# Performance work log

Measured on AMD Instinct MI355X. Metric: run time of the kernel, lower is better.

Reference implementation:

```python
import jax, jax.numpy as jnp
import numpy as np

D = 512
H = 4
HD = D // H
FF = 4 * D
B = 512
T = 128
EMA_K = 128
LOC_K = 4
DECAY = 0.9
STEP = 0.5 / np.sqrt(128 / 32)  # 0.25
EPS = 1e-5


def layernorm(x, g, b):
    mu = jnp.mean(x, axis=-1, keepdims=True)
    var = jnp.mean(jnp.square(x - mu), axis=-1, keepdims=True)
    return (x - mu) * jax.lax.rsqrt(var + EPS) * g + b


def dwconv_causal(x, w):
    # x: (B,T,D), w: (D,K); torch Conv1d(groups=D, padding=K-1) sliced to [:T]
    K = w.shape[1]
    xt = jnp.transpose(x, (0, 2, 1))  # (B,D,T)
    y = jax.lax.conv_general_dilated(
        xt, w[:, None, :], window_strides=(1,), padding=[(K - 1, 0)],
        feature_group_count=x.shape[-1], dimension_numbers=('NCT', 'OIT', 'NCT'))
    return jnp.transpose(y, (0, 2, 1))


def rope(qk, cos, sin):
    # qk: (B,H,T,HD)
    x1, x2 = jnp.split(qk, 2, axis=-1)
    rot = jnp.concatenate([-x2, x1], axis=-1)
    return qk * cos + rot * sin


def setup_inputs() -> dict:
    key = jax.random.key(0)
    ks = jax.random.split(key, 24)
    s = 0.02
    inp = {
        'parallel_repr': jax.random.normal(ks[0], (B, T, D), jnp.float32),
        'sequential_state': jax.random.normal(ks[1], (B, D), jnp.float32),
        'q_w': jax.random.normal(ks[2], (D, D), jnp.float32) * s,
        'q_b': jnp.zeros((D,), jnp.float32),
        'k_w': jax.random.normal(ks[3], (D, D), jnp.float32) * s,
        'k_b': jnp.zeros((D,), jnp.float32),
        'v_w': jax.random.normal(ks[4], (D, D), jnp.float32) * s,
        'v_b': jnp.zeros((D,), jnp.float32),
        'o_w': jax.random.normal(ks[5], (D, D), jnp.float32) * s,
        'o_b': jnp.zeros((D,), jnp.float32),
        'local_w': jax.random.normal(ks[6], (D, LOC_K), jnp.float32) * 0.1,
        'local_b': jax.random.normal(ks[7], (D,), jnp.float32) * 0.1,
        'delta_w': jax.random.normal(ks[8], (3 * D, D), jnp.float32) * s,
        'delta_b': jnp.zeros((D,), jnp.float32),
        'gate_w': jax.random.normal(ks[9], (3 * D, D), jnp.float32) * s,
        'gate_b': jnp.zeros((D,), jnp.float32),
        'dn_g': jnp.ones((D,), jnp.float32), 'dn_b': jnp.zeros((D,), jnp.float32),
        'ln1_g': jnp.ones((D,), jnp.float32), 'ln1_b': jnp.zeros((D,), jnp.float32),
        'ln2_g': jnp.ones((D,), jnp.float32), 'ln2_b': jnp.zeros((D,), jnp.float32),
        'ln3_g': jnp.ones((D,), jnp.float32), 'ln3_b': jnp.zeros((D,), jnp.float32),
        'ln4_g': jnp.ones((D,), jnp.float32), 'ln4_b': jnp.zeros((D,), jnp.float32),
        'seq_w': jax.random.normal(ks[10], (D, D), jnp.float32) * s,
        'seq_b': jnp.zeros((D,), jnp.float32),
        'ffn_w1': jax.random.normal(ks[11], (D, FF), jnp.float32) * s,
        'ffn_b1': jnp.zeros((FF,), jnp.float32),
        'ffn_w2': jax.random.normal(ks[12], (FF, D), jnp.float32) * s,
        'ffn_b2': jnp.zeros((D,), jnp.float32),
    }
    # EMA kernel: coefficient (1-d)*d^lag on x[t-lag]; stored flipped as in torch
    ema = (1.0 - DECAY) * DECAY ** jnp.arange(EMA_K, dtype=jnp.float32)
    inp['ema_w'] = jnp.broadcast_to(ema[::-1][None, :], (D, EMA_K))
    return inp


def reference(parallel_repr, sequential_state, q_w, q_b, k_w, k_b, v_w, v_b,
              o_w, o_b, local_w, local_b, delta_w, delta_b, gate_w, gate_b,
              dn_g, dn_b, ln1_g, ln1_b, ln2_g, ln2_b, ln3_g, ln3_b, ln4_g, ln4_b,
              seq_w, seq_b, ffn_w1, ffn_b1, ffn_w2, ffn_b2, ema_w):
    x = parallel_repr
    Bb, Tt, Dd = x.shape
    # --- RoPE causal attention ---
    inv_freq = 1.0 / (10000.0 ** (jnp.arange(0, HD, 2, dtype=jnp.float32) / HD))
    t = jnp.arange(Tt, dtype=jnp.float32)
    freqs = jnp.outer(t, inv_freq)                      # (T, HD/2)
    emb = jnp.concatenate([freqs, freqs], axis=-1)      # (T, HD)
    cos = jnp.cos(emb)[None, None]
    sin = jnp.sin(emb)[None, None]
    def heads(y):
        return jnp.transpose(y.reshape(Bb, Tt, H, HD), (0, 2, 1, 3))
    q = rope(heads(x @ q_w + q_b), cos, sin)
    k = rope(heads(x @ k_w + k_b), cos, sin)
    v = heads(x @ v_w + v_b)
    scores = jnp.einsum('bhtd,bhsd->bhts', q, k) / np.sqrt(HD)
    causal = jnp.tril(jnp.ones((Tt, Tt), dtype=bool))
    scores = jnp.where(causal, scores, jnp.float32(-1e9))
    attn = jax.nn.softmax(scores, axis=-1)
    attn_out = jnp.einsum('bhts,bhsd->bhtd', attn, v)
    attn_out = jnp.transpose(attn_out, (0, 2, 1, 3)).reshape(Bb, Tt, Dd)
    attn_out = attn_out @ o_w + o_b
    x1 = layernorm(x + attn_out, ln1_g, ln1_b)
    # --- depthwise causal convs ---
    local_hist = dwconv_causal(x1, local_w) + local_b
    global_sum = dwconv_causal(x1, ema_w)
    combined = jnp.concatenate([x1, local_hist, global_sum], axis=-1)  # (B,T,3D)
    deltas = jax.nn.sigmoid(combined @ gate_w + gate_b) * jnp.tanh(combined @ delta_w + delta_b)
    deltas = layernorm(deltas, dn_g, dn_b)
    acc = jnp.cumsum(deltas, axis=1) * STEP
    states = layernorm(sequential_state[:, None, :] + acc, ln3_g, ln3_b)
    seq_guidance = states @ seq_w + seq_b
    ffn_in = x1 + 0.3 * seq_guidance
    h = jax.nn.gelu(ffn_in @ ffn_w1 + ffn_b1, approximate=False)
    ffn_out = h @ ffn_w2 + ffn_b2
    out = layernorm(x1 + ffn_out, ln2_g, ln2_b)
    final_state = layernorm(states[:, -1, :], ln4_g, ln4_b)
    return out, final_state
```

## Files before the change

kernel.cpp:

```cpp
#include <hip/hip_runtime.h>
#include <cstddef>
#include <cstdint>

#define BB   512
#define TT   128
#define DD   512
#define HH   4
#define HDIM 128
#define FFD  2048
#define NROWS (BB * TT)
#define SLOT ((size_t)NROWS * DD)

typedef unsigned short u16;
typedef __bf16 bf16x8 __attribute__((ext_vector_type(8)));
typedef float  f32x4  __attribute__((ext_vector_type(4)));

__device__ __forceinline__ u16 f2b(float x) {
    union { float f; unsigned u; } v; v.f = x;
    unsigned r = v.u + 0x7FFFu + ((v.u >> 16) & 1u);
    return (u16)(r >> 16);
}
__device__ __forceinline__ float b2f(u16 u) {
    union { unsigned u; float f; } v; v.u = (unsigned)u << 16; return v.f;
}
__device__ __forceinline__ float fast_gelu(float v) {
    float t = v * (0.7978845608028654f + 0.0356774081f * v * v);
    float e = __expf(2.f * t);
    float th = 1.f - 2.f / (e + 1.f);
    return 0.5f * v * (1.f + th);
}
__device__ __forceinline__ void glds16(const void* g, void* l) {
    __builtin_amdgcn_global_load_lds(
        (const __attribute__((address_space(1))) void*)g,
        (__attribute__((address_space(3))) void*)l, 16, 0, 0);
}

template<int MODE>
__global__ __launch_bounds__(256)
void gemm128(const u16* __restrict__ A, const u16* __restrict__ BT,
             const float* __restrict__ bias, void* __restrict__ Cout, int ldc,
             const float* __restrict__ addsrc, void* __restrict__ aux,
             int K, int M)
{
    __shared__ u16 S[16384];
    const int tid = threadIdx.x;
    const int gx  = gridDim.x;
    const int nwg = gx * gridDim.y;
    int orig = blockIdx.y * gx + blockIdx.x;
    if ((nwg & 7) == 0) orig = (orig & 7) * (nwg >> 3) + (orig >> 3);
    const int row0 = (orig / gx) * 128;
    const int col0 = (orig % gx) * 128;

    const int lane = tid & 63;
    const int w    = tid >> 6;
    const int wr   = (w >> 1) * 64;
    const int wc   = (w & 1) * 64;
    const int fr   = lane & 15;
    const int kq   = lane >> 4;

    f32x4 acc[4][4];
#pragma unroll
    for (int m = 0; m < 4; ++m)
#pragma unroll
        for (int n = 0; n < 4; ++n) acc[m][n] = (f32x4){0.f, 0.f, 0.f, 0.f};

    const u16* agp[4]; const u16* bgp[4]; int dstoff[4];
#pragma unroll
    for (int j = 0; j < 4; ++j) {
        const int p   = w * 256 + j * 64 + lane;
        const int row = p >> 3;
        const int lc  = (p & 7) ^ (row & 7);
        agp[j] = A  + (size_t)(row0 + row) * K + lc * 8;
        bgp[j] = BT + (size_t)(col0 + row) * K + lc * 8;
        dstoff[j] = p * 8;
    }

    const int NKT = K >> 6;
    for (int kt = 0; kt < NKT; ++kt) {
        const int ko = kt * 64;
#pragma unroll
        for (int j = 0; j < 4; ++j) {
            glds16(agp[j] + ko, S + dstoff[j]);
            glds16(bgp[j] + ko, S + 8192 + dstoff[j]);
        }
        __syncthreads();
#pragma unroll
        for (int kk = 0; kk < 2; ++kk) {
            bf16x8 av[4], bv[4];
#pragma unroll
            for (int m = 0; m < 4; ++m) {
                const int r  = wr + m * 16 + fr;
                const int ch = (kk * 4 + kq) ^ (r & 7);
                av[m] = *(const bf16x8*)(S + r * 64 + ch * 8);
            }
#pragma unroll
            for (int n = 0; n < 4; ++n) {
                const int r  = wc + n * 16 + fr;
                const int ch = (kk * 4 + kq) ^ (r & 7);
                bv[n] = *(const bf16x8*)(S + 8192 + r * 64 + ch * 8);
            }
#pragma unroll
            for (int m = 0; m < 4; ++m)
#pragma unroll
                for (int n = 0; n < 4; ++n)
                    acc[m][n] = __builtin_amdgcn_mfma_f32_16x16x32_bf16(
                        av[m], bv[n], acc[m][n], 0, 0, 0);
        }
        __syncthreads();
    }

    if constexpr (MODE == 7) {
        if (col0 >= 1024) {
#pragma unroll
            for (int m = 0; m < 4; ++m)
#pragma unroll
                for (int j = 0; j < 4; ++j) {
                    const int tl = wr + m * 16 + (lane >> 4) * 4 + j;
#pragma unroll
                    for (int n = 0; n < 4; ++n) {
                        const int dc = wc + n * 16 + fr;
                        float v = acc[m][n][j] + bias[col0 + dc];
                        *(u16*)((char*)S + dc * 256 + ((tl * 2) ^ ((dc & 7) << 4))) = f2b(v);
                    }
                }
            __syncthreads();
            u16* dst = (u16*)aux + ((size_t)((row0 >> 7) * 4 + ((col0 - 1024) >> 7)) << 14);
#pragma unroll
            for (int i = 0; i < 8; ++i)
                *(uint4*)(dst + (size_t)(i * 256 + tid) * 8) =
                    *(const uint4*)((char*)S + (size_t)(i * 256 + tid) * 16);
        } else {
#pragma unroll
            for (int m = 0; m < 4; ++m)
#pragma unroll
                for (int j = 0; j < 4; ++j) {
                    const int r = row0 + wr + m * 16 + (lane >> 4) * 4 + j;
#pragma unroll
                    for (int n = 0; n < 4; ++n) {
                        const int c = col0 + wc + n * 16 + fr;
                        ((u16*)Cout)[(size_t)r * 1024 + c] = f2b(acc[m][n][j] + bias[c]);
                    }
                }
        }
    } else {
#pragma unroll
        for (int m = 0; m < 4; ++m) {
#pragma unroll
            for (int j = 0; j < 4; ++j) {
                const int r = row0 + wr + m * 16 + (lane >> 4) * 4 + j;
#pragma unroll
                for (int n = 0; n < 4; ++n) {
                    const int c = col0 + wc + n * 16 + fr;
                    float v = acc[m][n][j] + bias[c];
                    if constexpr (MODE == 2) {
                        ((u16*)Cout)[(size_t)r * ldc + c] =
                            f2b(addsrc[(size_t)r * M + c] + 0.3f * v);
                    } else if constexpr (MODE == 3) {
                        ((u16*)Cout)[(size_t)r * ldc + c] = f2b(fast_gelu(v));
                    } else if constexpr (MODE == 6) {
                        float pth = __shfl_xor(v, 1);
                        if ((fr & 1) == 0) {
                            float sg = 1.f / (1.f + __expf(-v));
                            float e  = __expf(2.f * pth);
                            float th = 1.f - 2.f / (e + 1.f);
                            ((u16*)Cout)[(size_t)r * ldc + (c >> 1)] = f2b(sg * th);
                        }
                    } else {
                        ((u16*)Cout)[(size_t)r * ldc + c] = f2b(v);
                    }
                }
            }
        }
    }
    (void)aux;
}

__global__ __launch_bounds__(256)
void wtrans_kernel(const float* __restrict__ W, u16* __restrict__ WT, int K, int M,
                   int rmul, int roff)
{
    __shared__ float t[32][33];
    const int m0 = blockIdx.x * 32;
    const int k0 = blockIdx.y * 32;
    const int tx = threadIdx.x;
    const int ty = threadIdx.y;
#pragma unroll
    for (int i = 0; i < 4; ++i) {
        int k = ty * 4 + i;
        t[k][tx] = W[(size_t)(k0 + k) * M + m0 + tx];
    }
    __syncthreads();
#pragma unroll
    for (int i = 0; i < 4; ++i) {
        int m = ty * 4 + i;
        WT[(size_t)((m0 + m) * rmul + roff) * K + k0 + tx] = f2b(t[tx][m]);
    }
}

__global__ void cast_f2b_kernel(const float* __restrict__ in, u16* __restrict__ out, size_t n4)
{
    size_t i = (size_t)blockIdx.x * blockDim.x + threadIdx.x;
    if (i >= n4) return;
    float4 v = reinterpret_cast<const float4*>(in)[i];
    union { u16 u[4]; uint2 d; } p;
    p.u[0] = f2b(v.x); p.u[1] = f2b(v.y); p.u[2] = f2b(v.z); p.u[3] = f2b(v.w);
    reinterpret_cast<uint2*>(out)[i] = p.d;
}

__global__ void rope_table_kernel(float* __restrict__ tabc, float* __restrict__ tabs)
{
    int idx = blockIdx.x * blockDim.x + threadIdx.x;
    if (idx >= TT * 64) return;
    int t = idx >> 6, j = idx & 63;
    float invf = expf(-(float)j * (9.210340371976184f / 64.f));
    float ang  = (float)t * invf;
    tabc[idx] = cosf(ang);
    tabs[idx] = sinf(ang);
}

__global__ void bias_build_kernel(const float* qb, const float* kb, const float* vb,
                                  const float* gb, const float* db,
                                  float* qkvb, float* gdb)
{
    int i = blockIdx.x * blockDim.x + threadIdx.x;
    if (i >= 512) return;
    qkvb[i] = qb[i]; qkvb[512 + i] = kb[i]; qkvb[1024 + i] = vb[i];
    gdb[2 * i] = gb[i]; gdb[2 * i + 1] = db[i];
}

__global__ __launch_bounds__(256)
void attn_mfma_kernel(const u16* __restrict__ QKg, const u16* __restrict__ VTg,
                      u16* __restrict__ Og,
                      const float* __restrict__ tabc, const float* __restrict__ tabs)
{
    __shared__ u16 SA[128 * 128];
    __shared__ u16 SB[128 * 128];
    const int h = blockIdx.x, b = blockIdx.y;
    const int tid  = threadIdx.x;
    const int lane = tid & 63;
    const int w    = tid >> 6;
    const int fr   = lane & 15;
    const int kq   = lane >> 4;
    const size_t baseq = ((size_t)(b * TT)) * 1024 + (size_t)h * HDIM;
    const size_t baseo = ((size_t)(b * TT)) * DD + (size_t)h * HDIM;

    {
        const int tg = tid >> 4;
        const int dg = tid & 15;
        const int j0 = (dg & 7) * 8;
        const bool hi = (dg & 8) != 0;
        for (int r = 0; r < 8; ++r) {
            const int t = r * 16 + tg;
            uint4 qv = *(const uint4*)(QKg + baseq + (size_t)t * 1024 + dg * 8);
            uint4 kv = *(const uint4*)(QKg + baseq + 512 + (size_t)t * 1024 + dg * 8);
            unsigned qa[4] = {qv.x, qv.y, qv.z, qv.w};
            unsigned ka[4] = {kv.x, kv.y, kv.z, kv.w};
            unsigned qb[4], kb[4];
#pragma unroll
            for (int i = 0; i < 4; ++i) {
                qb[i] = __shfl_xor((int)qa[i], 8);
                kb[i] = __shfl_xor((int)ka[i], 8);
            }
            const float* cp = tabc + t * 64 + j0;
            const float* sp = tabs + t * 64 + j0;
            u16 oq[8], ok[8];
#pragma unroll
            for (int e = 0; e < 8; ++e) {
                float fq = b2f((u16)(qa[e >> 1] >> ((e & 1) * 16)));
                float gq = b2f((u16)(qb[e >> 1] >> ((e & 1) * 16)));
                float fk = b2f((u16)(ka[e >> 1] >> ((e & 1) * 16)));
                float gk = b2f((u16)(kb[e >> 1] >> ((e & 1) * 16)));
                float c = cp[e], s = sp[e];
                oq[e] = f2b(hi ? fq * c + gq * s : fq * c - gq * s);
                ok[e] = f2b(hi ? fk * c + gk * s : fk * c - gk * s);
            }
            const int cb = (dg * 16) ^ ((t & 7) << 4);
            *(uint4*)((char*)SA + t * 256 + cb) = *(const uint4*)oq;
            *(uint4*)((char*)SB + t * 256 + cb) = *(const uint4*)ok;
        }
    }
    __syncthreads();

    f32x4 acc[2][8];
#pragma unroll
    for (int m = 0; m < 2; ++m)
#pragma unroll
        for (int n = 0; n < 8; ++n) acc[m][n] = (f32x4){0.f, 0.f, 0.f, 0.f};

    for (int k0 = 0; k0 < 128; k0 += 32) {
        const int cb = (k0 + kq * 8) * 2;
        bf16x8 af[2];
#pragma unroll
        for (int m = 0; m < 2; ++m) {
            const int row = w * 32 + m * 16 + fr;
            af[m] = *(const bf16x8*)((char*)SA + row * 256 + (cb ^ ((row & 7) << 4)));
        }
#pragma unroll
        for (int n = 0; n < 8; ++n) {
            const int row = n * 16 + fr;
            bf16x8 bf = *(const bf16x8*)((char*)SB + row * 256 + (cb ^ ((row & 7) << 4)));
            acc[0][n] = __builtin_amdgcn_mfma_f32_16x16x32_bf16(af[0], bf, acc[0][n], 0, 0, 0);
            acc[1][n] = __builtin_amdgcn_mfma_f32_16x16x32_bf16(af[1], bf, acc[1][n], 0, 0, 0);
        }
    }
    __syncthreads();

    {
        const u16* vsrc = VTg + ((size_t)(b * HH + h) << 14);
#pragma unroll
        for (int i = 0; i < 8; ++i)
            glds16(vsrc + (size_t)(i * 256 + tid) * 8,
                   SB + (size_t)(i * 256 + tid) * 8);
    }

    const float SC = 0.08838834764831845f;
#pragma unroll
    for (int m = 0; m < 2; ++m) {
#pragma unroll
        for (int j = 0; j < 4; ++j) {
            const int t = w * 32 + m * 16 + kq * 4 + j;
            float mx = -3.0e38f;
#pragma unroll
            for (int n = 0; n < 8; ++n) {
                const int s = n * 16 + fr;
                float v = acc[m][n][j];
                v = (s <= t) ? v * SC : -3.0e38f;
                acc[m][n][j] = v;
                mx = fmaxf(mx, v);
            }
            mx = fmaxf(mx, __shfl_xor(mx, 1));
            mx = fmaxf(mx, __shfl_xor(mx, 2));
            mx = fmaxf(mx, __shfl_xor(mx, 4));
            mx = fmaxf(mx, __shfl_xor(mx, 8));
            float sum = 0.f;
#pragma unroll
            for (int n = 0; n < 8; ++n) {
                float e = __expf(acc[m][n][j] - mx);
                acc[m][n][j] = e; sum += e;
            }
            sum += __shfl_xor(sum, 1); sum += __shfl_xor(sum, 2);
            sum += __shfl_xor(sum, 4); sum += __shfl_xor(sum, 8);
            const float inv = 1.f / sum;
#pragma unroll
            for (int n = 0; n < 8; ++n) {
                const int s = n * 16 + fr;
                *(u16*)((char*)SA + t * 256 + ((s * 2) ^ ((t & 7) << 4))) =
                    f2b(acc[m][n][j] * inv);
            }
        }
    }
    __syncthreads();

    f32x4 oa[2][8];
#pragma unroll
    for (int m = 0; m < 2; ++m)
#pragma unroll
        for (int n = 0; n < 8; ++n) oa[m][n] = (f32x4){0.f, 0.f, 0.f, 0.f};

    for (int k0 = 0; k0 < 128; k0 += 32) {
        const int cb = (k0 + kq * 8) * 2;
        bf16x8 pa[2];
#pragma unroll
        for (int m = 0; m < 2; ++m) {
            const int row = w * 32 + m * 16 + fr;
            pa[m] = *(const bf16x8*)((char*)SA + row * 256 + (cb ^ ((row & 7) << 4)));
        }
#pragma unroll
        for (int n = 0; n < 8; ++n) {
            const int row = n * 16 + fr;
            bf16x8 vb = *(const bf16x8*)((char*)SB + row * 256 + (cb ^ ((row & 7) << 4)));
            oa[0][n] = __builtin_amdgcn_mfma_f32_16x16x32_bf16(pa[0], vb, oa[0][n], 0, 0, 0);
            oa[1][n] = __builtin_amdgcn_mfma_f32_16x16x32_bf16(pa[1], vb, oa[1][n], 0, 0, 0);
        }
    }

#pragma unroll
    for (int m = 0; m < 2; ++m)
#pragma unroll
        for (int j = 0; j < 4; ++j) {
            const int t = w * 32 + m * 16 + kq * 4 + j;
            u16* orow = Og + baseo + (size_t)t * DD;
#pragma unroll
            for (int n = 0; n < 8; ++n)
                orow[n * 16 + fr] = f2b(oa[m][n][j]);
        }
}

__device__ __forceinline__ float2 blk_red512(float v, float (*red)[2], int tid)
{
    float s = v, ss = v * v;
#pragma unroll
    for (int off = 1; off < 64; off <<= 1) {
        s  += __shfl_xor(s, off);
        ss += __shfl_xor(ss, off);
    }
    if ((tid & 63) == 0) { red[tid >> 6][0] = s; red[tid >> 6][1] = ss; }
    __syncthreads();
    float S = 0.f, SS = 0.f;
#pragma unroll
    for (int w = 0; w < 8; ++w) { S += red[w][0]; SS += red[w][1]; }
    return make_float2(S, SS);
}

__global__ __launch_bounds__(512)
void ln1_chain_kernel(const float* __restrict__ x, const u16* __restrict__ oo,
                      const float* __restrict__ g, const float* __restrict__ bb,
                      const float* __restrict__ lw, const float* __restrict__ lb,
                      float* __restrict__ X1, u16* __restrict__ Cb)
{
    __shared__ float red[2][8][2];
    const int b = blockIdx.x, d = threadIdx.x;
    const float g_ = g[d], b_ = bb[d];
    const float w0 = lw[d * 4 + 0], w1 = lw[d * 4 + 1],
                w2 = lw[d * 4 + 2], w3 = lw[d * 4 + 3];
    const float lb_ = lb[d];
    const size_t rb = (size_t)b * TT;
    float h1 = 0.f, h2 = 0.f, h3 = 0.f, ema = 0.f;
    float v = x[(rb + 0) * DD + d] + b2f(oo[(rb + 0) * DD + d]);
    for (int t = 0; t < TT; ++t) {
        const int tn = (t < TT - 1) ? t + 1 : t;
        float vn = x[(rb + tn) * DD + d] + b2f(oo[(rb + tn) * DD + d]);
        float2 r = blk_red512(v, red[t & 1], d);
        float mu  = r.x * (1.f / DD);
        float var = r.y * (1.f / DD) - mu * mu;
        float x1v = (v - mu) * rsqrtf(var + 1e-5f) * g_ + b_;
        const size_t row = rb + t;
        X1[row * DD + d] = x1v;
        u16* crow = Cb + row * 1536;
        crow[d] = f2b(x1v);
        crow[512 + d]  = f2b(lb_ + w3 * x1v + w2 * h1 + w1 * h2 + w0 * h3);
        ema = 0.9f * ema + 0.1f * x1v;
        crow[1024 + d] = f2b(ema);
        h3 = h2; h2 = h1; h1 = x1v;
        v = vn;
    }
}

__global__ __launch_bounds__(512)
void state_chain_kernel(const u16* __restrict__ deltasB, const float* __restrict__ seqst,
                        const float* __restrict__ dng, const float* __restrict__ dnb,
                        const float* __restrict__ g3, const float* __restrict__ b3,
                        const float* __restrict__ g4, const float* __restrict__ b4,
                        u16* __restrict__ statesb, float* __restrict__ fstate)
{
    __shared__ float red[2][8][2];
    const int b = blockIdx.x, d = threadIdx.x;
    const float gd_ = dng[d], bd_ = dnb[d], g3_ = g3[d], b3_ = b3[d];
    const float seq = seqst[(size_t)b * DD + d];
    const size_t rb = (size_t)b * TT;
    float cum = 0.f;
    float v = b2f(deltasB[(rb + 0) * DD + d]);
    for (int t = 0; t < TT; ++t) {
        const int tn = (t < TT - 1) ? t + 1 : t;
        float vn = b2f(deltasB[(rb + tn) * DD + d]);
        float2 r0 = blk_red512(v, red[0], d);
        float mu  = r0.x * (1.f / DD);
        float var = r0.y * (1.f / DD) - mu * mu;
        float nd  = (v - mu) * rsqrtf(var + 1e-5f) * gd_ + bd_;
        cum += nd;
        float sv = seq + cum * 0.25f;
        float2 r1 = blk_red512(sv, red[1], d);
        mu  = r1.x * (1.f / DD);
        var = r1.y * (1.f / DD) - mu * mu;
        float o = (sv - mu) * rsqrtf(var + 1e-5f) * g3_ + b3_;
        statesb[(rb + t) * DD + d] = f2b(o);
        if (t == TT - 1) {
            float2 r2 = blk_red512(o, red[0], d);
            float mu4  = r2.x * (1.f / DD);
            float var4 = r2.y * (1.f / DD) - mu4 * mu4;
            fstate[(size_t)b * DD + d] = (o - mu4) * rsqrtf(var4 + 1e-5f) * g4[d] + b4[d];
        }
        v = vn;
    }
}

__global__ __launch_bounds__(256)
void ln2_kernel(const float* __restrict__ a, const u16* __restrict__ badd,
                const float* __restrict__ g, const float* __restrict__ bb,
                float* __restrict__ out)
{
    const int row = blockIdx.x;
    const int tid = threadIdx.x;
    const float* ap = a + (size_t)row * DD;
    const u16*   bp = badd + (size_t)row * DD;
    float v0 = ap[tid]       + b2f(bp[tid]);
    float v1 = ap[tid + 256] + b2f(bp[tid + 256]);
    float s  = v0 + v1;
    float ss = v0 * v0 + v1 * v1;
#pragma unroll
    for (int off = 1; off < 64; off <<= 1) {
        s  += __shfl_xor(s, off);
        ss += __shfl_xor(ss, off);
    }
    __shared__ float sm1[4], sm2[4];
    const int wid = tid >> 6;
    if ((tid & 63) == 0) { sm1[wid] = s; sm2[wid] = ss; }
    __syncthreads();
    s  = sm1[0] + sm1[1] + sm1[2] + sm1[3];
    ss = sm2[0] + sm2[1] + sm2[2] + sm2[3];
    const float mu  = s * (1.f / DD);
    const float var = ss * (1.f / DD) - mu * mu;
    const float r   = rsqrtf(var + 1e-5f);
    float* op = out + (size_t)row * DD;
    op[tid]       = (v0 - mu) * r * g[tid]       + bb[tid];
    op[tid + 256] = (v1 - mu) * r * g[tid + 256] + bb[tid + 256];
}

extern "C" void kernel_launch(void* const* d_in, const int* in_sizes, int n_in,
                              void* d_out, int out_size, void* d_ws, size_t ws_size,
                              hipStream_t stream)
{
    const float* x       = (const float*)d_in[0];
    const float* seqst   = (const float*)d_in[1];
    const float* q_w     = (const float*)d_in[2];
    const float* q_b     = (const float*)d_in[3];
    const float* k_w     = (const float*)d_in[4];
    const float* k_b     = (const float*)d_in[5];
    const float* v_w     = (const float*)d_in[6];
    const float* v_b     = (const float*)d_in[7];
    const float* o_w     = (const float*)d_in[8];
    const float* o_b     = (const float*)d_in[9];
    const float* local_w = (const float*)d_in[10];
    const float* local_b = (const float*)d_in[11];
    const float* delta_w = (const float*)d_in[12];
    const float* delta_b = (const float*)d_in[13];
    const float* gate_w  = (const float*)d_in[14];
    const float* gate_b  = (const float*)d_in[15];
    const float* dn_g    = (const float*)d_in[16];
    const float* dn_b    = (const float*)d_in[17];
    const float* ln1_g   = (const float*)d_in[18];
    const float* ln1_b   = (const float*)d_in[19];
    const float* ln2_g   = (const float*)d_in[20];
    const float* ln2_b   = (const float*)d_in[21];
    const float* ln3_g   = (const float*)d_in[22];
    const float* ln3_b   = (const float*)d_in[23];
    const float* ln4_g   = (const float*)d_in[24];
    const float* ln4_b   = (const float*)d_in[25];
    const float* seq_w   = (const float*)d_in[26];
    const float* seq_b   = (const float*)d_in[27];
    const float* ffn_w1  = (const float*)d_in[28];
    const float* ffn_b1  = (const float*)d_in[29];
    const float* ffn_w2  = (const float*)d_in[30];
    const float* ffn_b2  = (const float*)d_in[31];
    (void)in_sizes; (void)n_in; (void)out_size; (void)ws_size;

    float* out = (float*)d_out;
    char*  ws  = (char*)d_ws;
    const size_t MB = (size_t)1 << 20;

    u16*   xb      = (u16*)(ws + 0);
    u16*   QKb     = (u16*)(ws + 64 * MB);
    u16*   VTb     = (u16*)(ws + 192 * MB);
    u16*   attnb   = (u16*)(ws + 256 * MB);
    u16*   Oob     = (u16*)(ws + 0);
    u16*   Cb      = (u16*)(ws + 64 * MB);
    u16*   deltasB = (u16*)(ws + 256 * MB);
    u16*   statesb = (u16*)(ws + 320 * MB);
    u16*   ffn_inb = (u16*)(ws + 0);
    u16*   hb      = (u16*)(ws + 64 * MB);
    u16*   Fob     = (u16*)(ws + 320 * MB);
    u16*   WSq  = (u16*)(ws + 448 * MB);
    u16*   WSo  = (u16*)(ws + 450 * MB);
    u16*   WSgd = (u16*)(ws + 451 * MB);
    u16*   WSs  = (u16*)(ws + 455 * MB);
    u16*   WSf1 = (u16*)(ws + 456 * MB);
    u16*   WSf2 = (u16*)(ws + 458 * MB);
    float* qkvb = (float*)(ws + 460 * MB);
    float* gdb  = (float*)(ws + 461 * MB);

    float* X1     = out;
    float* tabc   = out + SLOT;
    float* tabs   = tabc + TT * 64;
    float* fstate = out + SLOT;

    const size_t NE = (size_t)NROWS * DD;

    rope_table_kernel<<<(TT * 64 + 255) / 256, 256, 0, stream>>>(tabc, tabs);
    cast_f2b_kernel<<<(unsigned)((NE / 4 + 255) / 256), 256, 0, stream>>>(x, xb, NE / 4);
    bias_build_kernel<<<2, 256, 0, stream>>>(q_b, k_b, v_b, gate_b, delta_b, qkvb, gdb);
    auto wt = [&](const float* W, u16* WT, int K, int M, int rmul, int roff) {
        wtrans_kernel<<<dim3(M / 32, K / 32), dim3(32, 8), 0, stream>>>(W, WT, K, M, rmul, roff);
    };
    wt(q_w, WSq, DD, DD, 1, 0);
    wt(k_w, WSq + (size_t)512 * DD, DD, DD, 1, 0);
    wt(v_w, WSq + (size_t)1024 * DD, DD, DD, 1, 0);
    wt(o_w, WSo, DD, DD, 1, 0);
    wt(gate_w,  WSgd, 3 * DD, DD, 2, 0);
    wt(delta_w, WSgd, 3 * DD, DD, 2, 1);
    wt(seq_w, WSs, DD, DD, 1, 0);
    wt(ffn_w1, WSf1, DD, FFD, 1, 0);
    wt(ffn_w2, WSf2, FFD, DD, 1, 0);

    gemm128<7><<<dim3(12, 512), 256, 0, stream>>>(
        xb, WSq, qkvb, QKb, 1024, nullptr, VTb, DD, 1536);

    attn_mfma_kernel<<<dim3(HH, BB), 256, 0, stream>>>(QKb, VTb, attnb, tabc, tabs);

    gemm128<4><<<dim3(4, 512), 256, 0, stream>>>(
        attnb, WSo, o_b, Oob, DD, nullptr, nullptr, DD, DD);

    ln1_chain_kernel<<<BB, 512, 0, stream>>>(x, Oob, ln1_g, ln1_b, local_w, local_b, X1, Cb);

    gemm128<6><<<dim3(8, 512), 256, 0, stream>>>(
        Cb, WSgd, gdb, deltasB, DD, nullptr, nullptr, 3 * DD, 1024);

    state_chain_kernel<<<BB, 512, 0, stream>>>(
        deltasB, seqst, dn_g, dn_b, ln3_g, ln3_b, ln4_g, ln4_b, statesb, fstate);

    gemm128<2><<<dim3(4, 512), 256, 0, stream>>>(
        statesb, WSs, seq_b, ffn_inb, DD, X1, nullptr, DD, DD);

    gemm128<3><<<dim3(16, 512), 256, 0, stream>>>(
        ffn_inb, WSf1, ffn_b1, hb, FFD, nullptr, nullptr, DD, FFD);
    gemm128<4><<<dim3(4, 512), 256, 0, stream>>>(
        hb, WSf2, ffn_b2, Fob, DD, nullptr, nullptr, FFD, DD);

    ln2_kernel<<<NROWS, 256, 0, stream>>>(X1, Fob, ln2_g, ln2_b, out);
}
```

Measured before the change: 1.761 ms.

## Drop fp32 X1 buffer, chunk FFN through small scratch, halve GEMM K-tile

The fp32 X1 intermediate is dropped. LN1 now reads the bf16 copy of x, and the residual paths read the bf16 x1 already stored in the concatenated Cb buffer, which cuts HBM traffic. The FFN up/down GEMMs run in four row chunks so the 2048-wide hidden activation stays in a smaller scratch region that may remain L2/MALL resident. The GEMM K-tile drops from 64 to 32, halving LDS use per block to raise occupancy, at the cost of twice as many barriers per K. The bf16 residuals lose some precision compared with fp32 x and x1.

```diff
diff --git a/kernel.cpp b/kernel.cpp
--- a/kernel.cpp
+++ b/kernel.cpp
@@ -39,10 +39,10 @@
 __global__ __launch_bounds__(256)
 void gemm128(const u16* __restrict__ A, const u16* __restrict__ BT,
              const float* __restrict__ bias, void* __restrict__ Cout, int ldc,
-             const float* __restrict__ addsrc, void* __restrict__ aux,
+             const void* __restrict__ addsrc, void* __restrict__ aux,
              int K, int M)
 {
-    __shared__ u16 S[16384];
+    __shared__ u16 S[(MODE == 7) ? 16384 : 8192];
     const int tid = threadIdx.x;
     const int gx  = gridDim.x;
     const int nwg = gx * gridDim.y;
@@ -64,48 +64,45 @@
 #pragma unroll
         for (int n = 0; n < 4; ++n) acc[m][n] = (f32x4){0.f, 0.f, 0.f, 0.f};
 
-    const u16* agp[4]; const u16* bgp[4]; int dstoff[4];
-#pragma unroll
-    for (int j = 0; j < 4; ++j) {
-        const int p   = w * 256 + j * 64 + lane;
-        const int row = p >> 3;
-        const int lc  = (p & 7) ^ (row & 7);
+    const u16* agp[2]; const u16* bgp[2]; int dstoff[2];
+#pragma unroll
+    for (int j = 0; j < 2; ++j) {
+        const int p   = w * 128 + j * 64 + lane;
+        const int row = p >> 2;
+        const int lc  = (p & 3) ^ (row & 3);
         agp[j] = A  + (size_t)(row0 + row) * K + lc * 8;
         bgp[j] = BT + (size_t)(col0 + row) * K + lc * 8;
         dstoff[j] = p * 8;
     }
 
-    const int NKT = K >> 6;
+    const int NKT = K >> 5;
     for (int kt = 0; kt < NKT; ++kt) {
-        const int ko = kt * 64;
-#pragma unroll
-        for (int j = 0; j < 4; ++j) {
+        const int ko = kt * 32;
+#pragma unroll
+        for (int j = 0; j < 2; ++j) {
             glds16(agp[j] + ko, S + dstoff[j]);
-            glds16(bgp[j] + ko, S + 8192 + dstoff[j]);
+            glds16(bgp[j] + ko, S + 4096 + dstoff[j]);
         }
         __syncthreads();
-#pragma unroll
-        for (int kk = 0; kk < 2; ++kk) {
-            bf16x8 av[4], bv[4];
-#pragma unroll
-            for (int m = 0; m < 4; ++m) {
-                const int r  = wr + m * 16 + fr;
-                const int ch = (kk * 4 + kq) ^ (r & 7);
-                av[m] = *(const bf16x8*)(S + r * 64 + ch * 8);
-            }
-#pragma unroll
-            for (int n = 0; n < 4; ++n) {
-                const int r  = wc + n * 16 + fr;
-                const int ch = (kk * 4 + kq) ^ (r & 7);
-                bv[n] = *(const bf16x8*)(S + 8192 + r * 64 + ch * 8);
-            }
-#pragma unroll
-            for (int m = 0; m < 4; ++m)
-#pragma unroll
-                for (int n = 0; n < 4; ++n)
-                    acc[m][n] = __builtin_amdgcn_mfma_f32_16x16x32_bf16(
-                        av[m], bv[n], acc[m][n], 0, 0, 0);
-        }
+        bf16x8 av[4], bv[4];
+#pragma unroll
+        for (int m = 0; m < 4; ++m) {
+            const int r  = wr + m * 16 + fr;
+            const int ch = kq ^ (r & 3);
+            av[m] = *(const bf16x8*)(S + r * 32 + ch * 8);
+        }
+#pragma unroll
+        for (int n = 0; n < 4; ++n) {
+            const int r  = wc + n * 16 + fr;
+            const int ch = kq ^ (r & 3);
+            bv[n] = *(const bf16x8*)(S + 4096 + r * 32 + ch * 8);
+        }
+#pragma unroll
+        for (int m = 0; m < 4; ++m)
+#pragma unroll
+            for (int n = 0; n < 4; ++n)
+                acc[m][n] = __builtin_amdgcn_mfma_f32_16x16x32_bf16(
+                    av[m], bv[n], acc[m][n], 0, 0, 0);
         __syncthreads();
     }
 
@@ -153,8 +150,8 @@
                     const int c = col0 + wc + n * 16 + fr;
                     float v = acc[m][n][j] + bias[c];
                     if constexpr (MODE == 2) {
-                        ((u16*)Cout)[(size_t)r * ldc + c] =
-                            f2b(addsrc[(size_t)r * M + c] + 0.3f * v);
+                        float xs = b2f(((const u16*)addsrc)[(size_t)r * M + c]);
+                        ((u16*)Cout)[(size_t)r * ldc + c] = f2b(xs + 0.3f * v);
                     } else if constexpr (MODE == 3) {
                         ((u16*)Cout)[(size_t)r * ldc + c] = f2b(fast_gelu(v));
                     } else if constexpr (MODE == 6) {
@@ -172,7 +169,7 @@
             }
         }
     }
-    (void)aux;
+    (void)aux; (void)addsrc;
 }
 
 __global__ __launch_bounds__(256)
@@ -403,10 +400,10 @@
 }
 
 __global__ __launch_bounds__(512)
-void ln1_chain_kernel(const float* __restrict__ x, const u16* __restrict__ oo,
+void ln1_chain_kernel(const u16* __restrict__ xb, const u16* __restrict__ oo,
                       const float* __restrict__ g, const float* __restrict__ bb,
                       const float* __restrict__ lw, const float* __restrict__ lb,
-                      float* __restrict__ X1, u16* __restrict__ Cb)
+                      u16* __restrict__ Cb)
 {
     __shared__ float red[2][8][2];
     const int b = blockIdx.x, d = threadIdx.x;
@@ -416,16 +413,15 @@
     const float lb_ = lb[d];
     const size_t rb = (size_t)b * TT;
     float h1 = 0.f, h2 = 0.f, h3 = 0.f, ema = 0.f;
-    float v = x[(rb + 0) * DD + d] + b2f(oo[(rb + 0) * DD + d]);
+    float v = b2f(xb[(rb + 0) * DD + d]) + b2f(oo[(rb + 0) * DD + d]);
     for (int t = 0; t < TT; ++t) {
         const int tn = (t < TT - 1) ? t + 1 : t;
-        float vn = x[(rb + tn) * DD + d] + b2f(oo[(rb + tn) * DD + d]);
+        float vn = b2f(xb[(rb + tn) * DD + d]) + b2f(oo[(rb + tn) * DD + d]);
         float2 r = blk_red512(v, red[t & 1], d);
         float mu  = r.x * (1.f / DD);
         float var = r.y * (1.f / DD) - mu * mu;
         float x1v = (v - mu) * rsqrtf(var + 1e-5f) * g_ + b_;
         const size_t row = rb + t;
-        X1[row * DD + d] = x1v;
         u16* crow = Cb + row * 1536;
         crow[d] = f2b(x1v);
         crow[512 + d]  = f2b(lb_ + w3 * x1v + w2 * h1 + w1 * h2 + w0 * h3);
@@ -475,16 +471,16 @@
 }
 
 __global__ __launch_bounds__(256)
-void ln2_kernel(const float* __restrict__ a, const u16* __restrict__ badd,
+void ln2_kernel(const u16* __restrict__ x1cb, const u16* __restrict__ fo,
                 const float* __restrict__ g, const float* __restrict__ bb,
                 float* __restrict__ out)
 {
     const int row = blockIdx.x;
     const int tid = threadIdx.x;
-    const float* ap = a + (size_t)row * DD;
-    const u16*   bp = badd + (size_t)row * DD;
-    float v0 = ap[tid]       + b2f(bp[tid]);
-    float v1 = ap[tid + 256] + b2f(bp[tid + 256]);
+    const u16* ap = x1cb + (size_t)row * 1536;
+    const u16* bp = fo   + (size_t)row * DD;
+    float v0 = b2f(ap[tid])       + b2f(bp[tid]);
+    float v1 = b2f(ap[tid + 256]) + b2f(bp[tid + 256]);
     float s  = v0 + v1;
     float ss = v0 * v0 + v1 * v1;
 #pragma unroll
@@ -552,12 +548,12 @@
     u16*   QKb     = (u16*)(ws + 64 * MB);
     u16*   VTb     = (u16*)(ws + 192 * MB);
     u16*   attnb   = (u16*)(ws + 256 * MB);
-    u16*   Oob     = (u16*)(ws + 0);
+    u16*   Oob     = (u16*)(ws + 320 * MB);
     u16*   Cb      = (u16*)(ws + 64 * MB);
     u16*   deltasB = (u16*)(ws + 256 * MB);
     u16*   statesb = (u16*)(ws + 320 * MB);
     u16*   ffn_inb = (u16*)(ws + 0);
-    u16*   hb      = (u16*)(ws + 64 * MB);
+    u16*   hb      = (u16*)(ws + 256 * MB);
     u16*   Fob     = (u16*)(ws + 320 * MB);
     u16*   WSq  = (u16*)(ws + 448 * MB);
     u16*   WSo  = (u16*)(ws + 450 * MB);
@@ -568,7 +564,6 @@
     float* qkvb = (float*)(ws + 460 * MB);
     float* gdb  = (float*)(ws + 461 * MB);
 
-    float* X1     = out;
     float* tabc   = out + SLOT;
     float* tabs   = tabc + TT * 64;
     float* fstate = out + SLOT;
@@ -599,7 +594,7 @@
     gemm128<4><<<dim3(4, 512), 256, 0, stream>>>(
         attnb, WSo, o_b, Oob, DD, nullptr, nullptr, DD, DD);
 
-    ln1_chain_kernel<<<BB, 512, 0, stream>>>(x, Oob, ln1_g, ln1_b, local_w, local_b, X1, Cb);
+    ln1_chain_kernel<<<BB, 512, 0, stream>>>(xb, Oob, ln1_g, ln1_b, local_w, local_b, Cb);
 
     gemm128<6><<<dim3(8, 512), 256, 0, stream>>>(
         Cb, WSgd, gdb, deltasB, DD, nullptr, nullptr, 3 * DD, 1024);
@@ -608,12 +603,19 @@
         deltasB, seqst, dn_g, dn_b, ln3_g, ln3_b, ln4_g, ln4_b, statesb, fstate);
 
     gemm128<2><<<dim3(4, 512), 256, 0, stream>>>(
-        statesb, WSs, seq_b, ffn_inb, DD, X1, nullptr, DD, DD);
-
-    gemm128<3><<<dim3(16, 512), 256, 0, stream>>>(
-        ffn_inb, WSf1, ffn_b1, hb, FFD, nullptr, nullptr, DD, FFD);
-    gemm128<4><<<dim3(4, 512), 256, 0, stream>>>(
-        hb, WSf2, ffn_b2, Fob, DD, nullptr, nullptr, FFD, DD);
-
-    ln2_kernel<<<NROWS, 256, 0, stream>>>(X1, Fob, ln2_g, ln2_b, out);
-}
+        statesb, WSs, seq_b, ffn_inb, DD, Cb, nullptr, DD, 1536);
+
+    {
+        const int CH = 16384;
+        for (int c = 0; c < 4; ++c) {
+            const u16* Ain = ffn_inb + (size_t)c * CH * DD;
+            u16* Cchunk    = Fob     + (size_t)c * CH * DD;
+            gemm128<3><<<dim3(16, CH / 128), 256, 0, stream>>>(
+                Ain, WSf1, ffn_b1, hb, FFD, nullptr, nullptr, DD, FFD);
+            gemm128<4><<<dim3(4, CH / 128), 256, 0, stream>>>(
+                hb, WSf2, ffn_b2, Cchunk, DD, nullptr, nullptr, FFD, DD);
+        }
+    }
+
+    ln2_kernel<<<NROWS, 256, 0, stream>>>(Cb, Fob, ln2_g, ln2_b, out);
+}
```

New measurement: 1.828 ms. 1.04x slower.
